# Kernel tuning notes

Hardware: AMD Instinct MI355X
Metric: run time of the kernel (lower is better)

The kernel has to match this reference:

```python
import jax, jax.numpy as jnp
import numpy as np

E = 1_000_000   # metapath instances (edges)
N = 100_000     # destination nodes
H = 8           # num_heads
D = 32          # out_dim
NUM_ETYPES = 3
ALPHA = 0.01    # leaky relu slope
ETYPES = [0, 1, 2]  # etypes_mapping is identity


def setup_inputs() -> dict:
    key = jax.random.key(0)
    k = jax.random.split(key, 6)
    # xavier_normal gain=1.414 for attn: std = gain*sqrt(2/(fan_in+fan_out))
    attn_std = 1.414 * np.sqrt(2.0 / (1 + D))
    return {
        "feat0": jax.random.normal(k[0], (E, D), jnp.float32),
        "feat1": jax.random.normal(k[1], (E, D), jnp.float32),
        "feat2": jax.random.normal(k[2], (E, D), jnp.float32),
        "r_vec": jax.random.normal(k[3], (NUM_ETYPES, D), jnp.float32),
        "attn": jax.random.normal(k[4], (1, H, D), jnp.float32) * attn_std,
        "dst": jax.random.randint(k[5], (E,), 0, N, dtype=jnp.int32),
        "num_nodes": N,
    }


def _l2norm(x):
    # torch F.normalize(p=2, dim=1)
    return x / jnp.maximum(jnp.linalg.norm(x, axis=1, keepdims=True), 1e-12)


def reference(feat0, feat1, feat2, r_vec, attn, dst, num_nodes):
    # --- TransE1 metapath-instance encoding ---
    feats = [_l2norm(feat0), _l2norm(feat1), _l2norm(feat2)]
    for i in range(len(ETYPES) - 1):
        feats[i] = feats[i] + r_vec[jnp.asarray(ETYPES[i:])].sum(axis=0)
    hidden = (feats[0] + feats[1] + feats[2]) / 3.0           # [E, D]
    # cat H copies then view(-1, H, D) == broadcast over head dim
    eft = jnp.broadcast_to(hidden[:, None, :], (hidden.shape[0], H, D))  # [E, H, D]

    # --- per-edge attention logits ---
    a = jnp.sum(eft * attn, axis=-1, keepdims=True)           # [E, H, 1]
    a = jax.nn.leaky_relu(a, negative_slope=ALPHA)

    # --- segment (edge) softmax over destination nodes ---
    m = jax.ops.segment_max(a, dst, num_segments=num_nodes)   # [N, H, 1]
    ex = jnp.exp(a - m[dst])
    s = jax.ops.segment_sum(ex, dst, num_segments=num_nodes)  # [N, H, 1]
    att = ex / s[dst]                                         # [E, H, 1]

    # --- weighted scatter-sum aggregation ---
    out = jax.ops.segment_sum(eft * att, dst, num_segments=num_nodes)  # [N, H, D]
    return out
```

## Files before the change

kernel.cpp:

```cpp
#include <hip/hip_runtime.h>
#include <hip/hip_fp16.h>

#define DD 32
#define HH 8
#define ALPHA 0.01f
#define REC 24
#define SCAN_T 256
#define SCAN_E 1024

__global__ __launch_bounds__(256) void k_zero(int* __restrict__ cnt, int N) {
    int i = blockIdx.x * 256 + threadIdx.x;
    if (i < N) cnt[i] = 0;
}

__global__ __launch_bounds__(256) void k_count(const int* __restrict__ dst, int E,
                                               int* __restrict__ cnt) {
    int e = blockIdx.x * 256 + threadIdx.x;
    if (e < E) atomicAdd(&cnt[dst[e]], 1);
}

__global__ __launch_bounds__(SCAN_T) void k_scan1(const int* __restrict__ cnt, int N,
                                                  int* __restrict__ bsum) {
    __shared__ int sh[SCAN_T];
    int t = threadIdx.x, b = blockIdx.x;
    int base = b * SCAN_E + t * 4;
    int s = 0;
    #pragma unroll
    for (int k = 0; k < 4; k++) { int i = base + k; if (i < N) s += cnt[i]; }
    sh[t] = s; __syncthreads();
    for (int off = SCAN_T / 2; off > 0; off >>= 1) {
        if (t < off) sh[t] += sh[t + off];
        __syncthreads();
    }
    if (t == 0) bsum[b] = sh[0];
}

__global__ __launch_bounds__(SCAN_T) void k_scan2(const int* __restrict__ bsum, int nb,
                                                  int* __restrict__ boff) {
    __shared__ int sh[SCAN_T];
    int t = threadIdx.x;
    int x = (t < nb) ? bsum[t] : 0;
    sh[t] = x; __syncthreads();
    for (int off = 1; off < SCAN_T; off <<= 1) {
        int v = (t >= off) ? sh[t - off] : 0;
        __syncthreads();
        sh[t] += v;
        __syncthreads();
    }
    if (t < nb) boff[t] = sh[t] - x;
}

__global__ __launch_bounds__(SCAN_T) void k_scan3(const int* __restrict__ cnt, int N, int E,
                                                  const int* __restrict__ boff,
                                                  int* __restrict__ row_ptr) {
    __shared__ int sh[SCAN_T];
    int t = threadIdx.x, b = blockIdx.x;
    int base = b * SCAN_E + t * 4;
    int c[4];
    #pragma unroll
    for (int k = 0; k < 4; k++) { int i = base + k; c[k] = (i < N) ? cnt[i] : 0; }
    int ts = c[0] + c[1] + c[2] + c[3];
    sh[t] = ts; __syncthreads();
    for (int off = 1; off < SCAN_T; off <<= 1) {
        int v = (t >= off) ? sh[t - off] : 0;
        __syncthreads();
        sh[t] += v;
        __syncthreads();
    }
    int rp = boff[b] + sh[t] - ts;
    int acc = 0;
    #pragma unroll
    for (int k = 0; k < 4; k++) {
        int i = base + k;
        if (i < N) row_ptr[i] = rp + acc;
        acc += c[k];
    }
    if (b == 0 && t == 0) row_ptr[N] = E;
}

__global__ __launch_bounds__(256) void k_edge(
    const float* __restrict__ f0, const float* __restrict__ f1, const float* __restrict__ f2,
    const float* __restrict__ rv, const float* __restrict__ attn,
    const int* __restrict__ dst, int E,
    const int* __restrict__ row_ptr, int* __restrict__ cnt,
    float* __restrict__ records)
{
    __shared__ float4 s_attn[HH * 8];
    __shared__ float s_R[DD];
    int t = threadIdx.x;
    if (t < 64) s_attn[t] = ((const float4*)attn)[t];
    if (t >= 64 && t < 96) {
        int d = t - 64;
        s_R[d] = rv[d] + 2.0f * (rv[DD + d] + rv[2 * DD + d]);
    }
    __syncthreads();

    int e = blockIdx.x * 256 + t;
    if (e >= E) return;

    int n = dst[e];
    int rp0 = row_ptr[n];
    int r = atomicAdd(&cnt[n], -1) - 1;

    const float4* p0 = (const float4*)(f0 + (size_t)e * DD);
    const float4* p1 = (const float4*)(f1 + (size_t)e * DD);
    const float4* p2 = (const float4*)(f2 + (size_t)e * DD);
    float4 a0[8], a1[8], a2[8];
    #pragma unroll
    for (int i = 0; i < 8; i++) a0[i] = p0[i];
    #pragma unroll
    for (int i = 0; i < 8; i++) a1[i] = p1[i];
    #pragma unroll
    for (int i = 0; i < 8; i++) a2[i] = p2[i];

    float s0 = 0.f, s1 = 0.f, s2 = 0.f;
    #pragma unroll
    for (int i = 0; i < 8; i++) {
        s0 += a0[i].x*a0[i].x + a0[i].y*a0[i].y + a0[i].z*a0[i].z + a0[i].w*a0[i].w;
        s1 += a1[i].x*a1[i].x + a1[i].y*a1[i].y + a1[i].z*a1[i].z + a1[i].w*a1[i].w;
        s2 += a2[i].x*a2[i].x + a2[i].y*a2[i].y + a2[i].z*a2[i].z + a2[i].w*a2[i].w;
    }
    float i0 = 1.0f / fmaxf(sqrtf(s0), 1e-12f);
    float i1 = 1.0f / fmaxf(sqrtf(s1), 1e-12f);
    float i2 = 1.0f / fmaxf(sqrtf(s2), 1e-12f);

    union HU { float4 v4[8]; float s[DD]; } h;
    #pragma unroll
    for (int i = 0; i < 8; i++) {
        h.v4[i].x = (a0[i].x*i0 + a1[i].x*i1 + a2[i].x*i2 + s_R[4*i+0]) * (1.0f/3.0f);
        h.v4[i].y = (a0[i].y*i0 + a1[i].y*i1 + a2[i].y*i2 + s_R[4*i+1]) * (1.0f/3.0f);
        h.v4[i].z = (a0[i].z*i0 + a1[i].z*i1 + a2[i].z*i2 + s_R[4*i+2]) * (1.0f/3.0f);
        h.v4[i].w = (a0[i].w*i0 + a1[i].w*i1 + a2[i].w*i2 + s_R[4*i+3]) * (1.0f/3.0f);
    }

    float ex[HH];
    #pragma unroll
    for (int q = 0; q < HH; q++) {
        float acc = 0.0f;
        #pragma unroll
        for (int i = 0; i < 8; i++) {
            float4 w = s_attn[q * 8 + i];
            float4 x = h.v4[i];
            acc += x.x*w.x + x.y*w.y + x.z*w.z + x.w*w.w;
        }
        float a = acc > 0.0f ? acc : ALPHA * acc;
        ex[q] = __expf(a);
    }

    union PU { __half2 h2[16]; float4 f4[4]; } u;
    #pragma unroll
    for (int i = 0; i < 16; i++) u.h2[i] = __floats2half2_rn(h.s[2*i], h.s[2*i+1]);

    float* recp = records + (size_t)(rp0 + r) * REC;
    float4* rq = (float4*)recp;
    rq[0] = make_float4(ex[0], ex[1], ex[2], ex[3]);
    rq[1] = make_float4(ex[4], ex[5], ex[6], ex[7]);
    #pragma unroll
    for (int i = 0; i < 4; i++) rq[2 + i] = u.f4[i];
}

__global__ __launch_bounds__(256) void k_agg(
    const float* __restrict__ records, const int* __restrict__ row_ptr,
    float* __restrict__ out, int N)
{
    int wid = threadIdx.x >> 6, lane = threadIdx.x & 63;
    int n = blockIdx.x * 4 + wid;
    if (n >= N) return;
    int r0 = row_ptr[n], r1 = row_ptr[n + 1];
    int deg = r1 - r0;
    int d = lane & 31;
    int hq = lane >> 5;

    float ssum[4] = {0.f, 0.f, 0.f, 0.f};
    float acc[4]  = {0.f, 0.f, 0.f, 0.f};
    const float* rec = records + (size_t)r0 * REC;

    int j = 0;
    for (; j + 1 < deg; j += 2) {
        const float* ra = rec + (size_t)j * REC;
        const float* rb = ra + REC;
        float4 xa = *(const float4*)(ra + hq * 4);
        float  ha = __half2float(((const __half*)(ra + 8))[d]);
        float4 xb = *(const float4*)(rb + hq * 4);
        float  hb = __half2float(((const __half*)(rb + 8))[d]);
        ssum[0] += xa.x; ssum[1] += xa.y; ssum[2] += xa.z; ssum[3] += xa.w;
        acc[0] += xa.x * ha; acc[1] += xa.y * ha; acc[2] += xa.z * ha; acc[3] += xa.w * ha;
        ssum[0] += xb.x; ssum[1] += xb.y; ssum[2] += xb.z; ssum[3] += xb.w;
        acc[0] += xb.x * hb; acc[1] += xb.y * hb; acc[2] += xb.z * hb; acc[3] += xb.w * hb;
    }
    if (j < deg) {
        const float* ra = rec + (size_t)j * REC;
        float4 xa = *(const float4*)(ra + hq * 4);
        float  ha = __half2float(((const __half*)(ra + 8))[d]);
        ssum[0] += xa.x; ssum[1] += xa.y; ssum[2] += xa.z; ssum[3] += xa.w;
        acc[0] += xa.x * ha; acc[1] += xa.y * ha; acc[2] += xa.z * ha; acc[3] += xa.w * ha;
    }

    size_t ob = (size_t)n * (HH * DD) + hq * 128 + d;
    #pragma unroll
    for (int k = 0; k < 4; k++) {
        float sv = ssum[k];
        float rr = sv > 0.0f ? 1.0f / sv : 0.0f;
        out[ob + k * 32] = acc[k] * rr;
    }
}

extern "C" void kernel_launch(void* const* d_in, const int* in_sizes, int n_in,
                              void* d_out, int out_size, void* d_ws, size_t ws_size,
                              hipStream_t stream)
{
    const float* f0   = (const float*)d_in[0];
    const float* f1   = (const float*)d_in[1];
    const float* f2   = (const float*)d_in[2];
    const float* rv   = (const float*)d_in[3];
    const float* attn = (const float*)d_in[4];
    const int*   dst  = (const int*)d_in[5];
    int E = in_sizes[0] / DD;
    int N = out_size / (HH * DD);
    float* out = (float*)d_out;

    auto al = [](size_t x) { return (x + 255) & ~(size_t)255; };
    char* w = (char*)d_ws;
    size_t off = 0;
    float* records = (float*)(w + off); off += al((size_t)E * REC * 4);
    int* row_ptr   = (int*)(w + off);   off += al(((size_t)N + 1) * 4);
    int* cnt       = (int*)(w + off);   off += al((size_t)N * 4);
    int* bsum      = (int*)(w + off);   off += al((size_t)SCAN_T * 4);
    int* boff      = (int*)(w + off);   off += al((size_t)SCAN_T * 4);
    (void)ws_size; (void)n_in;

    int nb = (N + SCAN_E - 1) / SCAN_E;

    k_zero<<<(N + 255) / 256, 256, 0, stream>>>(cnt, N);
    int gridE = (E + 255) / 256;
    k_count<<<gridE, 256, 0, stream>>>(dst, E, cnt);
    k_scan1<<<nb, SCAN_T, 0, stream>>>(cnt, N, bsum);
    k_scan2<<<1, SCAN_T, 0, stream>>>(bsum, nb, boff);
    k_scan3<<<nb, SCAN_T, 0, stream>>>(cnt, N, E, boff, row_ptr);
    k_edge<<<gridE, 256, 0, stream>>>(f0, f1, f2, rv, attn, dst, E, row_ptr, cnt, records);
    k_agg<<<(N + 3) / 4, 256, 0, stream>>>(records, row_ptr, out, N);
}
```

Before: 563.0 us.

## Fuse edge encoding into per-node aggregation via CSR edge-id indirection

Replaces the per-edge kernel that wrote sorted 96-byte records (exp logits plus fp16 hidden) with a small fill kernel that writes only the edge id into CSR order. A fused per-node kernel then gathers the three feature rows per edge through that indirection, computes norms and head logits with warp shuffles, and accumulates the softmax numerator and denominator directly. This removes the record write and read traffic and the fp16 rounding. In exchange the features are gathered randomly as 128-byte rows, and each edge needs many more shuffle reductions.

```diff
diff --git a/kernel.cpp b/kernel.cpp
--- a/kernel.cpp
+++ b/kernel.cpp
@@ -1,10 +1,8 @@
 #include <hip/hip_runtime.h>
-#include <hip/hip_fp16.h>
 
 #define DD 32
 #define HH 8
 #define ALPHA 0.01f
-#define REC 24
 #define SCAN_T 256
 #define SCAN_E 1024
 
@@ -78,130 +76,86 @@
     if (b == 0 && t == 0) row_ptr[N] = E;
 }
 
-__global__ __launch_bounds__(256) void k_edge(
+__global__ __launch_bounds__(256) void k_fill(const int* __restrict__ dst, int E,
+                                              const int* __restrict__ row_ptr,
+                                              int* __restrict__ cnt, int* __restrict__ eid) {
+    int e = blockIdx.x * 256 + threadIdx.x;
+    if (e >= E) return;
+    int n = dst[e];
+    int r = atomicAdd(&cnt[n], -1) - 1;
+    eid[row_ptr[n] + r] = e;
+}
+
+__global__ __launch_bounds__(256) void k_fused(
     const float* __restrict__ f0, const float* __restrict__ f1, const float* __restrict__ f2,
     const float* __restrict__ rv, const float* __restrict__ attn,
-    const int* __restrict__ dst, int E,
-    const int* __restrict__ row_ptr, int* __restrict__ cnt,
-    float* __restrict__ records)
-{
-    __shared__ float4 s_attn[HH * 8];
-    __shared__ float s_R[DD];
-    int t = threadIdx.x;
-    if (t < 64) s_attn[t] = ((const float4*)attn)[t];
-    if (t >= 64 && t < 96) {
-        int d = t - 64;
-        s_R[d] = rv[d] + 2.0f * (rv[DD + d] + rv[2 * DD + d]);
-    }
-    __syncthreads();
-
-    int e = blockIdx.x * 256 + t;
-    if (e >= E) return;
-
-    int n = dst[e];
-    int rp0 = row_ptr[n];
-    int r = atomicAdd(&cnt[n], -1) - 1;
-
-    const float4* p0 = (const float4*)(f0 + (size_t)e * DD);
-    const float4* p1 = (const float4*)(f1 + (size_t)e * DD);
-    const float4* p2 = (const float4*)(f2 + (size_t)e * DD);
-    float4 a0[8], a1[8], a2[8];
-    #pragma unroll
-    for (int i = 0; i < 8; i++) a0[i] = p0[i];
-    #pragma unroll
-    for (int i = 0; i < 8; i++) a1[i] = p1[i];
-    #pragma unroll
-    for (int i = 0; i < 8; i++) a2[i] = p2[i];
-
-    float s0 = 0.f, s1 = 0.f, s2 = 0.f;
-    #pragma unroll
-    for (int i = 0; i < 8; i++) {
-        s0 += a0[i].x*a0[i].x + a0[i].y*a0[i].y + a0[i].z*a0[i].z + a0[i].w*a0[i].w;
-        s1 += a1[i].x*a1[i].x + a1[i].y*a1[i].y + a1[i].z*a1[i].z + a1[i].w*a1[i].w;
-        s2 += a2[i].x*a2[i].x + a2[i].y*a2[i].y + a2[i].z*a2[i].z + a2[i].w*a2[i].w;
-    }
-    float i0 = 1.0f / fmaxf(sqrtf(s0), 1e-12f);
-    float i1 = 1.0f / fmaxf(sqrtf(s1), 1e-12f);
-    float i2 = 1.0f / fmaxf(sqrtf(s2), 1e-12f);
-
-    union HU { float4 v4[8]; float s[DD]; } h;
-    #pragma unroll
-    for (int i = 0; i < 8; i++) {
-        h.v4[i].x = (a0[i].x*i0 + a1[i].x*i1 + a2[i].x*i2 + s_R[4*i+0]) * (1.0f/3.0f);
-        h.v4[i].y = (a0[i].y*i0 + a1[i].y*i1 + a2[i].y*i2 + s_R[4*i+1]) * (1.0f/3.0f);
-        h.v4[i].z = (a0[i].z*i0 + a1[i].z*i1 + a2[i].z*i2 + s_R[4*i+2]) * (1.0f/3.0f);
-        h.v4[i].w = (a0[i].w*i0 + a1[i].w*i1 + a2[i].w*i2 + s_R[4*i+3]) * (1.0f/3.0f);
-    }
-
-    float ex[HH];
-    #pragma unroll
-    for (int q = 0; q < HH; q++) {
-        float acc = 0.0f;
-        #pragma unroll
-        for (int i = 0; i < 8; i++) {
-            float4 w = s_attn[q * 8 + i];
-            float4 x = h.v4[i];
-            acc += x.x*w.x + x.y*w.y + x.z*w.z + x.w*w.w;
-        }
-        float a = acc > 0.0f ? acc : ALPHA * acc;
-        ex[q] = __expf(a);
-    }
-
-    union PU { __half2 h2[16]; float4 f4[4]; } u;
-    #pragma unroll
-    for (int i = 0; i < 16; i++) u.h2[i] = __floats2half2_rn(h.s[2*i], h.s[2*i+1]);
-
-    float* recp = records + (size_t)(rp0 + r) * REC;
-    float4* rq = (float4*)recp;
-    rq[0] = make_float4(ex[0], ex[1], ex[2], ex[3]);
-    rq[1] = make_float4(ex[4], ex[5], ex[6], ex[7]);
-    #pragma unroll
-    for (int i = 0; i < 4; i++) rq[2 + i] = u.f4[i];
-}
-
-__global__ __launch_bounds__(256) void k_agg(
-    const float* __restrict__ records, const int* __restrict__ row_ptr,
+    const int* __restrict__ row_ptr, const int* __restrict__ eid,
     float* __restrict__ out, int N)
 {
     int wid = threadIdx.x >> 6, lane = threadIdx.x & 63;
     int n = blockIdx.x * 4 + wid;
     if (n >= N) return;
-    int r0 = row_ptr[n], r1 = row_ptr[n + 1];
-    int deg = r1 - r0;
     int d = lane & 31;
     int hq = lane >> 5;
 
-    float ssum[4] = {0.f, 0.f, 0.f, 0.f};
-    float acc[4]  = {0.f, 0.f, 0.f, 0.f};
-    const float* rec = records + (size_t)r0 * REC;
+    float att_q[HH];
+    #pragma unroll
+    for (int q = 0; q < HH; q++) att_q[q] = attn[q * DD + d];
+    float Rd = rv[d] + 2.0f * (rv[DD + d] + rv[2 * DD + d]);
 
-    int j = 0;
-    for (; j + 1 < deg; j += 2) {
-        const float* ra = rec + (size_t)j * REC;
-        const float* rb = ra + REC;
-        float4 xa = *(const float4*)(ra + hq * 4);
-        float  ha = __half2float(((const __half*)(ra + 8))[d]);
-        float4 xb = *(const float4*)(rb + hq * 4);
-        float  hb = __half2float(((const __half*)(rb + 8))[d]);
-        ssum[0] += xa.x; ssum[1] += xa.y; ssum[2] += xa.z; ssum[3] += xa.w;
-        acc[0] += xa.x * ha; acc[1] += xa.y * ha; acc[2] += xa.z * ha; acc[3] += xa.w * ha;
-        ssum[0] += xb.x; ssum[1] += xb.y; ssum[2] += xb.z; ssum[3] += xb.w;
-        acc[0] += xb.x * hb; acc[1] += xb.y * hb; acc[2] += xb.z * hb; acc[3] += xb.w * hb;
-    }
-    if (j < deg) {
-        const float* ra = rec + (size_t)j * REC;
-        float4 xa = *(const float4*)(ra + hq * 4);
-        float  ha = __half2float(((const __half*)(ra + 8))[d]);
-        ssum[0] += xa.x; ssum[1] += xa.y; ssum[2] += xa.z; ssum[3] += xa.w;
-        acc[0] += xa.x * ha; acc[1] += xa.y * ha; acc[2] += xa.z * ha; acc[3] += xa.w * ha;
+    int r0 = row_ptr[n], r1 = row_ptr[n + 1];
+    int deg = r1 - r0;
+
+    float num[HH], den[HH];
+    #pragma unroll
+    for (int q = 0; q < HH; q++) { num[q] = 0.f; den[q] = 0.f; }
+
+    for (int j = 0; j < deg; j += 2) {
+        int idx = j + hq;
+        bool valid = idx < deg;
+        int e = eid[r0 + (valid ? idx : 0)];
+        size_t off = (size_t)e * DD + d;
+        float x0 = f0[off], x1 = f1[off], x2 = f2[off];
+
+        float s0 = x0 * x0, s1 = x1 * x1, s2 = x2 * x2;
+        #pragma unroll
+        for (int o = 16; o >= 1; o >>= 1) {
+            s0 += __shfl_xor(s0, o, 32);
+            s1 += __shfl_xor(s1, o, 32);
+            s2 += __shfl_xor(s2, o, 32);
+        }
+        float i0 = 1.0f / fmaxf(sqrtf(s0), 1e-12f);
+        float i1 = 1.0f / fmaxf(sqrtf(s1), 1e-12f);
+        float i2 = 1.0f / fmaxf(sqrtf(s2), 1e-12f);
+        float h = (x0 * i0 + x1 * i1 + x2 * i2 + Rd) * (1.0f / 3.0f);
+
+        float ex[HH];
+        #pragma unroll
+        for (int q = 0; q < HH; q++) {
+            float p = h * att_q[q];
+            #pragma unroll
+            for (int o = 16; o >= 1; o >>= 1) p += __shfl_xor(p, o, 32);
+            float a = p > 0.f ? p : ALPHA * p;
+            ex[q] = valid ? __expf(a) : 0.f;
+        }
+        float hv = valid ? h : 0.f;
+        #pragma unroll
+        for (int q = 0; q < HH; q++) { den[q] += ex[q]; num[q] += ex[q] * hv; }
     }
 
-    size_t ob = (size_t)n * (HH * DD) + hq * 128 + d;
+    #pragma unroll
+    for (int q = 0; q < HH; q++) {
+        num[q] += __shfl_xor(num[q], 32, 64);
+        den[q] += __shfl_xor(den[q], 32, 64);
+    }
+
+    size_t ob = (size_t)n * (HH * DD);
     #pragma unroll
     for (int k = 0; k < 4; k++) {
-        float sv = ssum[k];
-        float rr = sv > 0.0f ? 1.0f / sv : 0.0f;
-        out[ob + k * 32] = acc[k] * rr;
+        int q = hq * 4 + k;
+        float dv = den[q];
+        float rr = dv > 0.f ? 1.0f / dv : 0.f;
+        out[ob + (size_t)q * DD + d] = num[q] * rr;
     }
 }
 
@@ -222,21 +176,21 @@
     auto al = [](size_t x) { return (x + 255) & ~(size_t)255; };
     char* w = (char*)d_ws;
     size_t off = 0;
-    float* records = (float*)(w + off); off += al((size_t)E * REC * 4);
-    int* row_ptr   = (int*)(w + off);   off += al(((size_t)N + 1) * 4);
-    int* cnt       = (int*)(w + off);   off += al((size_t)N * 4);
-    int* bsum      = (int*)(w + off);   off += al((size_t)SCAN_T * 4);
-    int* boff      = (int*)(w + off);   off += al((size_t)SCAN_T * 4);
+    int* eid     = (int*)(w + off); off += al((size_t)E * 4);
+    int* row_ptr = (int*)(w + off); off += al(((size_t)N + 1) * 4);
+    int* cnt     = (int*)(w + off); off += al((size_t)N * 4);
+    int* bsum    = (int*)(w + off); off += al((size_t)SCAN_T * 4);
+    int* boff    = (int*)(w + off); off += al((size_t)SCAN_T * 4);
     (void)ws_size; (void)n_in;
 
     int nb = (N + SCAN_E - 1) / SCAN_E;
+    int gridE = (E + 255) / 256;
 
     k_zero<<<(N + 255) / 256, 256, 0, stream>>>(cnt, N);
-    int gridE = (E + 255) / 256;
     k_count<<<gridE, 256, 0, stream>>>(dst, E, cnt);
     k_scan1<<<nb, SCAN_T, 0, stream>>>(cnt, N, bsum);
     k_scan2<<<1, SCAN_T, 0, stream>>>(bsum, nb, boff);
     k_scan3<<<nb, SCAN_T, 0, stream>>>(cnt, N, E, boff, row_ptr);
-    k_edge<<<gridE, 256, 0, stream>>>(f0, f1, f2, rv, attn, dst, E, row_ptr, cnt, records);
-    k_agg<<<(N + 3) / 4, 256, 0, stream>>>(records, row_ptr, out, N);
+    k_fill<<<gridE, 256, 0, stream>>>(dst, E, row_ptr, cnt, eid);
+    k_fused<<<(N + 3) / 4, 256, 0, stream>>>(f0, f1, f2, rv, attn, row_ptr, eid, out, N);
 }
```

After: 679.4 us. +20.7%, slower.
